# Kernel tuning notes

Measured on AMD Instinct MI355X. Metric: run time of the kernel, lower is better.

The kernel has to match this reference:

```python
import jax, jax.numpy as jnp
import numpy as np

B, BOND, N, ATOM, UNITS = 256, 5, 128, 64, 128


def setup_inputs() -> dict:
    key = jax.random.key(0)
    k1, k2, k3 = jax.random.split(key, 3)
    adjacency = jax.random.uniform(k1, (B, BOND, N, N), dtype=jnp.float32)
    features = jax.random.normal(k2, (B, N, ATOM), dtype=jnp.float32)
    # per-sample unique kernel: (global_batch, bond_dim, atom_dim, units)
    kernel = jax.random.normal(k3, (B, BOND, ATOM, UNITS), dtype=jnp.float32) * 0.05
    return {"adjacency": adjacency, "features": features, "kernel": kernel}


def reference(adjacency, features, kernel):
    # aggregate neighbors per bond type: [B, bond, N, atom]
    x = jnp.einsum('bemn,bnd->bemd', adjacency, features)
    # per-sample, per-bond linear transform: [B, bond, N, units]
    x = jnp.einsum('bemd,bedu->bemu', x, kernel)
    # reduce over bond types, then activation: [B, N, units]
    return jax.nn.relu(jnp.sum(x, axis=1))
```

## Files before the change

### kernel.cpp

```cpp
#include <hip/hip_runtime.h>


typedef __attribute__((ext_vector_type(8))) short s8v;
typedef __attribute__((ext_vector_type(4))) float f4v;

__device__ __forceinline__ short f2bf(float f) {
    unsigned u = __builtin_bit_cast(unsigned, f);
    u += 0x7FFFu + ((u >> 16) & 1u);
    return (short)(u >> 16);
}

__global__ __launch_bounds__(512, 2)
void rgc_kernel(const float* __restrict__ adj,
                const float* __restrict__ feat,
                const float* __restrict__ ker,
                float* __restrict__ out)
{
    __shared__ __align__(16) short featT[64][136];
    __shared__ __align__(16) short kerT[2][128][72];
    __shared__ __align__(16) short YB[128][72];

    const int b    = blockIdx.x;
    const int tid  = threadIdx.x;
    const int w    = tid >> 6;
    const int lane = tid & 63;
    const int c16  = lane & 15;
    const int quad = lane >> 4;

    const float* adjB  = adj  + (size_t)b * (5 * 128 * 128);
    const float* featB = feat + (size_t)b * (128 * 64);
    const float* kerB  = ker  + (size_t)b * (5 * 64 * 128);
    float*       outB  = out  + (size_t)b * (128 * 128);

    {
        f4v fv[4];
        #pragma unroll
        for (int i = 0; i < 4; ++i)
            fv[i] = *(const f4v*)(featB + (i * 512 + tid) * 4);
        #pragma unroll
        for (int i = 0; i < 4; ++i) {
            int g = i * 512 + tid;
            int n = g >> 4, d0 = (g & 15) << 2;
            #pragma unroll
            for (int j = 0; j < 4; ++j)
                featT[d0 + j][n] = f2bf(fv[i][j]);
        }
    }
    {
        f4v kv[4];
        #pragma unroll
        for (int i = 0; i < 4; ++i)
            kv[i] = *(const f4v*)(kerB + (i * 512 + tid) * 4);
        #pragma unroll
        for (int i = 0; i < 4; ++i) {
            int g = i * 512 + tid;
            int d = g >> 5, u0 = (g & 31) << 2;
            #pragma unroll
            for (int j = 0; j < 4; ++j)
                kerT[0][u0 + j][d] = f2bf(kv[i][j]);
        }
    }
    __syncthreads();

    f4v oacc[8] = {};

    for (int e = 0; e < 5; ++e) {
        const float* ap = adjB + e * (128 * 128) + (16 * w + c16) * 128 + 8 * quad;
        f4v a0[4], a1[4];
        #pragma unroll
        for (int k16 = 0; k16 < 4; ++k16) {
            a0[k16] = *(const f4v*)(ap + 32 * k16);
            a1[k16] = *(const f4v*)(ap + 32 * k16 + 4);
        }
        f4v kv[4];
        const int en = e + 1;
        if (en < 5) {
            #pragma unroll
            for (int i = 0; i < 4; ++i)
                kv[i] = *(const f4v*)(kerB + en * (64 * 128) + (i * 512 + tid) * 4);
        }

        f4v yacc[4] = {};
        #pragma unroll
        for (int k16 = 0; k16 < 4; ++k16) {
            s8v af;
            #pragma unroll
            for (int j = 0; j < 4; ++j) af[j] = f2bf(a0[k16][j]);
            #pragma unroll
            for (int j = 0; j < 4; ++j) af[4 + j] = f2bf(a1[k16][j]);
            #pragma unroll
            for (int d16 = 0; d16 < 4; ++d16) {
                s8v bf = *(const s8v*)&featT[16 * d16 + c16][32 * k16 + 8 * quad];
                yacc[d16] = __builtin_amdgcn_mfma_f32_16x16x32_bf16(af, bf, yacc[d16], 0, 0, 0);
            }
        }

        #pragma unroll
        for (int d16 = 0; d16 < 4; ++d16)
            #pragma unroll
            for (int r = 0; r < 4; ++r)
                YB[16 * w + 4 * quad + r][16 * d16 + c16] = f2bf(yacc[d16][r]);

        if (en < 5) {
            #pragma unroll
            for (int i = 0; i < 4; ++i) {
                int g = i * 512 + tid;
                int d = g >> 5, u0 = (g & 31) << 2;
                #pragma unroll
                for (int j = 0; j < 4; ++j)
                    kerT[en & 1][u0 + j][d] = f2bf(kv[i][j]);
            }
        }

        {
            const int buf = e & 1;
            s8v afr0 = *(const s8v*)&YB[16 * w + c16][8 * quad];
            s8v afr1 = *(const s8v*)&YB[16 * w + c16][32 + 8 * quad];
            #pragma unroll
            for (int u16 = 0; u16 < 8; ++u16) {
                s8v b0 = *(const s8v*)&kerT[buf][16 * u16 + c16][8 * quad];
                s8v b1 = *(const s8v*)&kerT[buf][16 * u16 + c16][32 + 8 * quad];
                oacc[u16] = __builtin_amdgcn_mfma_f32_16x16x32_bf16(afr0, b0, oacc[u16], 0, 0, 0);
                oacc[u16] = __builtin_amdgcn_mfma_f32_16x16x32_bf16(afr1, b1, oacc[u16], 0, 0, 0);
            }
        }
        __syncthreads();
    }

    #pragma unroll
    for (int u16 = 0; u16 < 8; ++u16)
        #pragma unroll
        for (int r = 0; r < 4; ++r)
            outB[(16 * w + 4 * quad + r) * 128 + 16 * u16 + c16] = fmaxf(oacc[u16][r], 0.f);
}

extern "C" void kernel_launch(void* const* d_in, const int* in_sizes, int n_in,
                              void* d_out, int out_size, void* d_ws, size_t ws_size,
                              hipStream_t stream)
{
    const float* adj  = (const float*)d_in[0];
    const float* feat = (const float*)d_in[1];
    const float* ker  = (const float*)d_in[2];
    rgc_kernel<<<256, 512, 0, stream>>>(adj, feat, ker, (float*)d_out);
}
```

Baseline: 172.1 us.

## Split each sample across four blocks and stream kernel weights directly from global

The grid goes from one 512-thread block per sample to four 256-thread blocks, each owning 32 output rows. Waves are split across rows and output-column halves. The shared-memory transposed kernel buffer and the per-bond block barriers are removed. Each wave now loads kernel weights straight from global memory with strided scalar loads and converts them to bf16 in registers. This raises parallelism and removes synchronisation, but increases redundant global/L2 traffic for the kernel and feature tensors.

```diff
diff --git a/kernel.cpp b/kernel.cpp
--- a/kernel.cpp
+++ b/kernel.cpp
@@ -10,19 +10,21 @@
     return (short)(u >> 16);
 }
 
-__global__ __launch_bounds__(512, 2)
+__global__ __launch_bounds__(256, 4)
 void rgc_kernel(const float* __restrict__ adj,
                 const float* __restrict__ feat,
                 const float* __restrict__ ker,
                 float* __restrict__ out)
 {
     __shared__ __align__(16) short featT[64][136];
-    __shared__ __align__(16) short kerT[2][128][72];
-    __shared__ __align__(16) short YB[128][72];
+    __shared__ __align__(16) short YB[4][16][72];
 
-    const int b    = blockIdx.x;
+    const int b    = blockIdx.x >> 2;
+    const int rg   = blockIdx.x & 3;
     const int tid  = threadIdx.x;
     const int w    = tid >> 6;
+    const int mw   = w >> 1;
+    const int uw   = w & 1;
     const int lane = tid & 63;
     const int c16  = lane & 15;
     const int quad = lane >> 4;
@@ -33,51 +35,35 @@
     float*       outB  = out  + (size_t)b * (128 * 128);
 
     {
-        f4v fv[4];
+        f4v fv[8];
         #pragma unroll
-        for (int i = 0; i < 4; ++i)
-            fv[i] = *(const f4v*)(featB + (i * 512 + tid) * 4);
+        for (int i = 0; i < 8; ++i)
+            fv[i] = *(const f4v*)(featB + (i * 256 + tid) * 4);
         #pragma unroll
-        for (int i = 0; i < 4; ++i) {
-            int g = i * 512 + tid;
+        for (int i = 0; i < 8; ++i) {
+            int g = i * 256 + tid;
             int n = g >> 4, d0 = (g & 15) << 2;
             #pragma unroll
             for (int j = 0; j < 4; ++j)
                 featT[d0 + j][n] = f2bf(fv[i][j]);
         }
     }
-    {
-        f4v kv[4];
-        #pragma unroll
-        for (int i = 0; i < 4; ++i)
-            kv[i] = *(const f4v*)(kerB + (i * 512 + tid) * 4);
-        #pragma unroll
-        for (int i = 0; i < 4; ++i) {
-            int g = i * 512 + tid;
-            int d = g >> 5, u0 = (g & 31) << 2;
-            #pragma unroll
-            for (int j = 0; j < 4; ++j)
-                kerT[0][u0 + j][d] = f2bf(kv[i][j]);
-        }
-    }
     __syncthreads();
 
-    f4v oacc[8] = {};
+    const int rowS = 32 * rg + 16 * mw;
+    const float* ap0 = adjB + (rowS + c16) * 128 + 8 * quad;
+    const float* kp0 = kerB + (8 * quad) * 128 + 64 * uw + c16;
+    short (*YBw)[72] = YB[w];
+
+    f4v oacc[4] = {};
 
     for (int e = 0; e < 5; ++e) {
-        const float* ap = adjB + e * (128 * 128) + (16 * w + c16) * 128 + 8 * quad;
+        const float* ap = ap0 + e * (128 * 128);
         f4v a0[4], a1[4];
         #pragma unroll
         for (int k16 = 0; k16 < 4; ++k16) {
             a0[k16] = *(const f4v*)(ap + 32 * k16);
             a1[k16] = *(const f4v*)(ap + 32 * k16 + 4);
-        }
-        f4v kv[4];
-        const int en = e + 1;
-        if (en < 5) {
-            #pragma unroll
-            for (int i = 0; i < 4; ++i)
-                kv[i] = *(const f4v*)(kerB + en * (64 * 128) + (i * 512 + tid) * 4);
         }
 
         f4v yacc[4] = {};
@@ -99,39 +85,30 @@
         for (int d16 = 0; d16 < 4; ++d16)
             #pragma unroll
             for (int r = 0; r < 4; ++r)
-                YB[16 * w + 4 * quad + r][16 * d16 + c16] = f2bf(yacc[d16][r]);
+                YBw[4 * quad + r][16 * d16 + c16] = f2bf(yacc[d16][r]);
+        s8v y0 = *(const s8v*)&YBw[c16][8 * quad];
+        s8v y1 = *(const s8v*)&YBw[c16][32 + 8 * quad];
 
-        if (en < 5) {
+        const float* kp = kp0 + e * (64 * 128);
+        #pragma unroll
+        for (int u16 = 0; u16 < 4; ++u16) {
+            s8v b0, b1;
             #pragma unroll
-            for (int i = 0; i < 4; ++i) {
-                int g = i * 512 + tid;
-                int d = g >> 5, u0 = (g & 31) << 2;
-                #pragma unroll
-                for (int j = 0; j < 4; ++j)
-                    kerT[en & 1][u0 + j][d] = f2bf(kv[i][j]);
+            for (int j = 0; j < 8; ++j) {
+                b0[j] = f2bf(kp[j * 128 + 16 * u16]);
+                b1[j] = f2bf(kp[(32 + j) * 128 + 16 * u16]);
             }
+            oacc[u16] = __builtin_amdgcn_mfma_f32_16x16x32_bf16(y0, b0, oacc[u16], 0, 0, 0);
+            oacc[u16] = __builtin_amdgcn_mfma_f32_16x16x32_bf16(y1, b1, oacc[u16], 0, 0, 0);
         }
-
-        {
-            const int buf = e & 1;
-            s8v afr0 = *(const s8v*)&YB[16 * w + c16][8 * quad];
-            s8v afr1 = *(const s8v*)&YB[16 * w + c16][32 + 8 * quad];
-            #pragma unroll
-            for (int u16 = 0; u16 < 8; ++u16) {
-                s8v b0 = *(const s8v*)&kerT[buf][16 * u16 + c16][8 * quad];
-                s8v b1 = *(const s8v*)&kerT[buf][16 * u16 + c16][32 + 8 * quad];
-                oacc[u16] = __builtin_amdgcn_mfma_f32_16x16x32_bf16(afr0, b0, oacc[u16], 0, 0, 0);
-                oacc[u16] = __builtin_amdgcn_mfma_f32_16x16x32_bf16(afr1, b1, oacc[u16], 0, 0, 0);
-            }
-        }
-        __syncthreads();
     }
 
     #pragma unroll
-    for (int u16 = 0; u16 < 8; ++u16)
+    for (int u16 = 0; u16 < 4; ++u16)
         #pragma unroll
         for (int r = 0; r < 4; ++r)
-            outB[(16 * w + 4 * quad + r) * 128 + 16 * u16 + c16] = fmaxf(oacc[u16][r], 0.f);
+            outB[(rowS + 4 * quad + r) * 128 + 64 * uw + 16 * u16 + c16] =
+                fmaxf(oacc[u16][r], 0.f);
 }
 
 extern "C" void kernel_launch(void* const* d_in, const int* in_sizes, int n_in,
@@ -141,5 +118,5 @@
     const float* adj  = (const float*)d_in[0];
     const float* feat = (const float*)d_in[1];
     const float* ker  = (const float*)d_in[2];
-    rgc_kernel<<<256, 512, 0, stream>>>(adj, feat, ker, (float*)d_out);
+    rgc_kernel<<<1024, 256, 0, stream>>>(adj, feat, ker, (float*)d_out);
 }
```

Measured after the change: 192.9 us. 1.12x slower.
